# Kernel tuning notes

Measured on AMD Instinct MI355X. Metric: run time of the kernel, lower is better.

The kernel has to match this reference:

```python
import jax, jax.numpy as jnp
import numpy as np

B, T, A_DIM, Z_DIM, K = 128, 80, 32, 64, 16


def setup_inputs() -> dict:
    key = jax.random.key(0)
    k1, k2, k3, k4 = jax.random.split(key, 4)
    obs = jax.random.normal(k1, (B, T, A_DIM), jnp.float32)
    alpha_logits = jax.random.normal(k2, (B, T, K), jnp.float32)
    # torch init: A = eye(z) repeated K times; small noise keeps 80-step recursion stable
    A_K = jnp.eye(Z_DIM, dtype=jnp.float32)[None] + 0.005 * jax.random.normal(k3, (K, Z_DIM, Z_DIM), jnp.float32)
    # torch init: C = 0.05 * randn
    C_K = 0.05 * jax.random.normal(k4, (K, A_DIM, Z_DIM), jnp.float32)
    return {"obs": obs, "alpha_logits": alpha_logits, "A_K": A_K, "C_K": C_K}


def _kalman(obs, A, C):
    # obs [B,T,a], A [B,T,z,z], C [B,T,a,z]
    Bq, Tq, a_dim = obs.shape
    z_dim = A.shape[-1]
    dt = obs.dtype
    Q = 0.08 * jnp.eye(z_dim, dtype=dt)
    R = 0.03 * jnp.eye(a_dim, dtype=dt)
    I = jnp.eye(z_dim, dtype=dt)

    obs_t = jnp.swapaxes(obs, 0, 1)          # [T,B,a]
    A_t = jnp.swapaxes(A, 0, 1)              # [T,B,z,z]
    C_t = jnp.swapaxes(C, 0, 1)              # [T,B,a,z]
    A_next = jnp.concatenate([A_t[1:], A_t[-1:]], axis=0)  # A[t+1]; last unused

    mu0 = jnp.zeros((Bq, z_dim), dt)
    sig0 = jnp.broadcast_to(20.0 * I, (Bq, z_dim, z_dim))

    def filt_step(carry, inp):
        mu_p, sig_p, mu_prev = carry
        At, Anx, Ct, y = inp
        CtT = jnp.swapaxes(Ct, -1, -2)
        S = Ct @ sig_p @ CtT + R                       # [B,a,a]
        Kg = sig_p @ CtT @ jnp.linalg.inv(S)            # [B,z,a]
        Amu = jnp.einsum('bij,bj->bi', At, mu_prev)     # A_t mu_{t-1}
        err = y - jnp.einsum('bij,bj->bi', Ct, Amu)
        mu_f = Amu + jnp.einsum('bij,bj->bi', Kg, err)
        sig_f = (I - Kg @ Ct) @ sig_p
        mu_pn = jnp.einsum('bij,bj->bi', Anx, mu_f)     # prediction with A_{t+1}
        sig_pn = Anx @ sig_f @ jnp.swapaxes(Anx, -1, -2) + Q
        return (mu_pn, sig_pn, mu_f), (mu_f, sig_f, mu_p, sig_p)

    _, (mu_f, sig_f, mu_p, sig_p) = jax.lax.scan(
        filt_step, (mu0, sig0, mu0), (A_t, A_next, C_t, obs_t))

    def smooth_step(carry, inp):
        mu_s, sig_s = carry
        mf, sf, Anx, mpn, spn = inp
        J = sf @ jnp.swapaxes(Anx, -1, -2) @ jnp.linalg.inv(spn)
        mu = mf + jnp.einsum('bij,bj->bi', J, mu_s - mpn)
        sig = sf + J @ (sig_s - spn) @ jnp.swapaxes(J, -1, -2)
        return (mu, sig), (mu, sig)

    init = (mu_f[-1], sig_f[-1])
    _, (mu_sm, sig_sm) = jax.lax.scan(
        smooth_step, init,
        (mu_f[:-1], sig_f[:-1], A_t[1:], mu_p[1:], sig_p[1:]),
        reverse=True)
    mu_sm = jnp.concatenate([mu_sm, mu_f[-1:]], axis=0)
    sig_sm = jnp.concatenate([sig_sm, sig_f[-1:]], axis=0)
    return jnp.swapaxes(mu_sm, 0, 1), jnp.swapaxes(sig_sm, 0, 1)  # [B,T,z], [B,T,z,z]


def reference(obs, alpha_logits, A_K, C_K):
    w = jax.nn.softmax(alpha_logits, axis=-1)                # [B,T,K]
    A = jnp.einsum('btk,kij->btij', w, A_K)                  # [B,T,z,z]
    C = jnp.einsum('btk,kij->btij', w, C_K)                  # [B,T,a,z]
    return _kalman(obs, A, C)
```

## Files before the change

### kernel.cpp

```cpp
#include <hip/hip_runtime.h>

#define B_ 128
#define T_ 80
#define AD 32
#define ZD 64
#define KD 16
#define S8 68
#define S4 34

template<int KL, int AS, int BS, bool ATRANS>
__device__ __forceinline__ void mm64(const float* __restrict__ Pa, const float* __restrict__ Qb,
                                     float acc[2][4], int r2, int c4)
{
#pragma unroll 8
    for (int k = 0; k < KL; k++) {
        float aA, aB;
        if (ATRANS) { aA = Pa[k * AS + r2];   aB = Pa[k * AS + r2 + 1]; }
        else        { aA = Pa[r2 * AS + k];   aB = Pa[(r2 + 1) * AS + k]; }
        const float4 bv = *(const float4*)&Qb[k * BS + c4];
        acc[0][0] += aA * bv.x; acc[0][1] += aA * bv.y; acc[0][2] += aA * bv.z; acc[0][3] += aA * bv.w;
        acc[1][0] += aB * bv.x; acc[1][1] += aB * bv.y; acc[1][2] += aB * bv.z; acc[1][3] += aB * bv.w;
    }
}

__global__ __launch_bounds__(512, 2)
void kvae_kernel(const float* __restrict__ obs, const float* __restrict__ logits,
                 const float* __restrict__ AK, const float* __restrict__ CK,
                 float* __restrict__ out)
{
    __shared__ __align__(16) float W[T_ * KD];
    __shared__ __align__(16) float Am[ZD * S8];
    __shared__ __align__(16) float At[ZD * S8];
    __shared__ __align__(16) float SP[ZD * S8];
    __shared__ __align__(16) float SF[ZD * S8];
    __shared__ __align__(16) float Mm[ZD * S8];
    __shared__ __align__(16) float Pool[9792];
    __shared__ __align__(16) float y_s[32];
    __shared__ __align__(16) float mup[64];
    __shared__ __align__(16) float muf[64];
    __shared__ __align__(16) float mus[64];
    __shared__ __align__(16) float mpn[64];
    __shared__ __align__(16) float dv[64];

    float* T1 = Pool;
    float* CM = Pool + 2176;
    float* CT = Pool + 4352;
    float* U_ = Pool + 6528;
    float* S_ = Pool + 8704;
    float* Xb = Pool;
    float* SG = Pool + 4352;

    const int tid = threadIdx.x;
    const int b   = blockIdx.x;

    const int r16 = tid >> 4;
    const int cg  = tid & 15;
    const int c4  = cg << 2;
    const int c2  = cg << 1;
    const int r2  = r16 << 1;
    const int i64 = tid >> 3;
    const int c8  = (tid & 7) << 3;

    const float* obs_b = obs    + (size_t)b * T_ * AD;
    const float* lg_b  = logits + (size_t)b * T_ * KD;
    float* omu = out + (size_t)b * T_ * ZD;
    float* osg = out + (size_t)B_ * T_ * ZD + (size_t)b * T_ * ZD * ZD;
    const float4* AK4 = (const float4*)AK;
    const float4* CK4 = (const float4*)CK;

    auto mixA_full = [&](int tt) {
#pragma unroll
        for (int rr = 0; rr < 2; rr++) {
            int r = r2 + rr;
            float4 a = make_float4(0.f, 0.f, 0.f, 0.f);
#pragma unroll
            for (int k = 0; k < KD; k++) {
                float wk = W[tt * KD + k];
                float4 v = AK4[k * 1024 + r * 16 + cg];
                a.x += wk * v.x; a.y += wk * v.y; a.z += wk * v.z; a.w += wk * v.w;
            }
            *(float4*)&Am[r * S8 + c4] = a;
            At[(c4 + 0) * S8 + r] = a.x; At[(c4 + 1) * S8 + r] = a.y;
            At[(c4 + 2) * S8 + r] = a.z; At[(c4 + 3) * S8 + r] = a.w;
        }
    };
    auto mixC_full = [&](int tt) {
        float4 a = make_float4(0.f, 0.f, 0.f, 0.f);
#pragma unroll
        for (int k = 0; k < KD; k++) {
            float wk = W[tt * KD + k];
            float4 v = CK4[k * 512 + r16 * 16 + cg];
            a.x += wk * v.x; a.y += wk * v.y; a.z += wk * v.z; a.w += wk * v.w;
        }
        *(float4*)&CM[r16 * S8 + c4] = a;
        CT[(c4 + 0) * S4 + r16] = a.x; CT[(c4 + 1) * S4 + r16] = a.y;
        CT[(c4 + 2) * S4 + r16] = a.z; CT[(c4 + 3) * S4 + r16] = a.w;
    };

    if (tid < T_) {
        float l[KD]; float mx = -1e30f;
#pragma unroll
        for (int k = 0; k < KD; k++) { l[k] = lg_b[tid * KD + k]; mx = fmaxf(mx, l[k]); }
        float s = 0.f;
#pragma unroll
        for (int k = 0; k < KD; k++) { l[k] = expf(l[k] - mx); s += l[k]; }
        float inv = 1.0f / s;
#pragma unroll
        for (int k = 0; k < KD; k++) W[tid * KD + k] = l[k] * inv;
    }
#pragma unroll
    for (int rr = 0; rr < 2; rr++) {
        int r = r2 + rr;
#pragma unroll
        for (int j = 0; j < 4; j++) SP[r * S8 + c4 + j] = (r == c4 + j) ? 20.0f : 0.0f;
    }
    if (tid < ZD) mup[tid] = 0.0f;
    __syncthreads();

    for (int t = 0; t < T_; t++) {
        if (t < T_ - 1) mixA_full(t + 1);
        mixC_full(t);
        if (tid < AD) y_s[tid] = obs_b[t * AD + tid];
        __syncthreads();

        {
            float a0 = 0, a1 = 0, a2 = 0, a3 = 0;
            const float* pa = CM + r16 * S8;
#pragma unroll 8
            for (int k = 0; k < ZD; k++) {
                float a = pa[k];
                float4 bv = *(const float4*)&SP[k * S8 + c4];
                a0 += a * bv.x; a1 += a * bv.y; a2 += a * bv.z; a3 += a * bv.w;
            }
            T1[r16 * S8 + c4 + 0] = a0; T1[r16 * S8 + c4 + 1] = a1;
            T1[r16 * S8 + c4 + 2] = a2; T1[r16 * S8 + c4 + 3] = a3;
        }
        __syncthreads();

        float4 ur; float ue = 0.f;
        {
            float a0 = 0, a1 = 0;
            const float* pa = T1 + r16 * S8;
#pragma unroll 8
            for (int k = 0; k < ZD; k++) {
                float a = pa[k];
                float2 bv = *(const float2*)&CT[k * S4 + c2];
                a0 += a * bv.x; a1 += a * bv.y;
            }
            if (r16 == c2)     a0 += 0.03f;
            if (r16 == c2 + 1) a1 += 0.03f;
            S_[r16 * S4 + c2] = a0; S_[r16 * S4 + c2 + 1] = a1;
            ur = *(const float4*)&T1[r16 * S8 + c4];
            if (cg == 15) {
                float s = 0.f;
                const float* pc = CM + r16 * S8;
#pragma unroll 8
                for (int k = 0; k < ZD; k++) s += pc[k] * mup[k];
                ue = y_s[r16] - s;
            }
            if (r16 < 2) {
                *(float4*)&U_[r16 * S8 + c4] = ur;
                if (cg == 15) U_[r16 * S8 + 64] = ue;
            }
        }
        __syncthreads();

#pragma unroll 1
        for (int j = 0; j < 16; j++) {
            const int p0 = 2 * j, p1 = p0 + 1;
            const int i = r16;
            const float f0 = S_[i * S4 + p0], f1 = S_[i * S4 + p1];
            const float qa = S_[p0 * S4 + p0], qb = S_[p0 * S4 + p1];
            const float qc = S_[p1 * S4 + p0], qd = S_[p1 * S4 + p1];
            const float l0x = S_[p0 * S4 + c2], l0y = S_[p0 * S4 + c2 + 1];
            const float l1x = S_[p1 * S4 + c2], l1y = S_[p1 * S4 + c2 + 1];
            const float4 r0 = *(const float4*)&U_[p0 * S8 + c4];
            const float4 r1 = *(const float4*)&U_[p1 * S8 + c4];
            float e0 = 0.f, e1 = 0.f;
            if (cg == 15) { e0 = U_[p0 * S8 + 64]; e1 = U_[p1 * S8 + 64]; }
            __syncthreads();
            const float dinv = 1.0f / (qa * qd - qb * qc);
            const float i00 =  qd * dinv, i01 = -qb * dinv;
            const float i10 = -qc * dinv, i11 =  qa * dinv;
            const float n0x = i00 * l0x + i01 * l1x, n0y = i00 * l0y + i01 * l1y;
            const float n1x = i10 * l0x + i11 * l1x, n1y = i10 * l0y + i11 * l1y;
            float4 m0, m1;
            m0.x = i00 * r0.x + i01 * r1.x; m0.y = i00 * r0.y + i01 * r1.y;
            m0.z = i00 * r0.z + i01 * r1.z; m0.w = i00 * r0.w + i01 * r1.w;
            m1.x = i10 * r0.x + i11 * r1.x; m1.y = i10 * r0.y + i11 * r1.y;
            m1.z = i10 * r0.z + i11 * r1.z; m1.w = i10 * r0.w + i11 * r1.w;
            const float me0 = i00 * e0 + i01 * e1, me1 = i10 * e0 + i11 * e1;
            if (i == p0) {
                S_[i * S4 + c2] = n0x; S_[i * S4 + c2 + 1] = n0y;
                ur = m0; if (cg == 15) ue = me0;
            } else if (i == p1) {
                S_[i * S4 + c2] = n1x; S_[i * S4 + c2 + 1] = n1y;
                ur = m1; if (cg == 15) ue = me1;
            } else {
                S_[i * S4 + c2]     -= f0 * n0x + f1 * n1x;
                S_[i * S4 + c2 + 1] -= f0 * n0y + f1 * n1y;
                ur.x -= f0 * m0.x + f1 * m1.x; ur.y -= f0 * m0.y + f1 * m1.y;
                ur.z -= f0 * m0.z + f1 * m1.z; ur.w -= f0 * m0.w + f1 * m1.w;
                if (cg == 15) ue -= f0 * me0 + f1 * me1;
            }
            if (j < 15 && (i == p0 + 2 || i == p0 + 3)) {
                *(float4*)&U_[i * S8 + c4] = ur;
                if (cg == 15) U_[i * S8 + 64] = ue;
            }
            __syncthreads();
        }
        *(float4*)&U_[r16 * S8 + c4] = ur;
        if (cg == 15) U_[r16 * S8 + 64] = ue;
        __syncthreads();

        {
            float acc[2][4] = {};
            mm64<AD, S8, S8, true>(T1, U_, acc, r2, c4);
            float* og = osg + (size_t)t * ZD * ZD;
#pragma unroll
            for (int rr = 0; rr < 2; rr++) {
                int r = r2 + rr;
                float4 sp = *(const float4*)&SP[r * S8 + c4];
                float4 v;
                v.x = sp.x - acc[rr][0]; v.y = sp.y - acc[rr][1];
                v.z = sp.z - acc[rr][2]; v.w = sp.w - acc[rr][3];
                *(float4*)&SF[r * S8 + c4] = v;
                *(float4*)(og + r * ZD + c4) = v;
            }
        }
        if (tid < ZD) {
            float s = 0.f;
#pragma unroll
            for (int k = 0; k < AD; k++) s += T1[k * S8 + tid] * U_[k * S8 + 64];
            float v = mup[tid] + s;
            muf[tid] = v;
            omu[t * ZD + tid] = v;
        }
        __syncthreads();

        if (t < T_ - 1) {
            {
                float acc[2][4] = {};
                mm64<ZD, S8, S8, false>(Am, SF, acc, r2, c4);
#pragma unroll
                for (int rr = 0; rr < 2; rr++)
                    *(float4*)&Mm[(r2 + rr) * S8 + c4] =
                        make_float4(acc[rr][0], acc[rr][1], acc[rr][2], acc[rr][3]);
            }
            __syncthreads();
            {
                float acc[2][4] = {};
                mm64<ZD, S8, S8, false>(Mm, At, acc, r2, c4);
#pragma unroll
                for (int rr = 0; rr < 2; rr++) {
                    int r = r2 + rr;
#pragma unroll
                    for (int j = 0; j < 4; j++)
                        SP[r * S8 + c4 + j] = acc[rr][j] + ((r == c4 + j) ? 0.08f : 0.0f);
                }
            }
            if (tid >= 448) {
                int i = tid - 448;
                float s = 0.f;
                const float* pa = Am + i * S8;
#pragma unroll 8
                for (int k = 0; k < ZD; k++) s += pa[k] * muf[k];
                mup[i] = s;
            }
            __syncthreads();
        }
    }

#pragma unroll
    for (int rr = 0; rr < 2; rr++) {
        int r = r2 + rr;
        *(float4*)&SG[r * S8 + c4] = *(const float4*)&SF[r * S8 + c4];
    }
    if (tid < ZD) mus[tid] = muf[tid];
    __syncthreads();

    for (int t = T_ - 2; t >= 0; t--) {
        mixA_full(t + 1);
        {
            const float4* og4 = (const float4*)(osg + (size_t)t * ZD * ZD);
#pragma unroll
            for (int rr = 0; rr < 2; rr++) {
                int r = r2 + rr;
                *(float4*)&SF[r * S8 + c4] = og4[r * 16 + cg];
            }
        }
        if (tid >= 448) muf[tid - 448] = omu[t * ZD + (tid - 448)];
        __syncthreads();

        {
            float acc[2][4] = {};
            mm64<ZD, S8, S8, false>(Am, SF, acc, r2, c4);
#pragma unroll
            for (int rr = 0; rr < 2; rr++) {
                int r = r2 + rr;
                float4 v = make_float4(acc[rr][0], acc[rr][1], acc[rr][2], acc[rr][3]);
                *(float4*)&Mm[r * S8 + c4] = v;
                *(float4*)&Xb[r * S8 + c4] = v;
            }
        }
        if (tid >= 448) {
            int i = tid - 448;
            float s = 0.f;
            const float* pa = Am + i * S8;
#pragma unroll 8
            for (int k = 0; k < ZD; k++) s += pa[k] * muf[k];
            mpn[i] = s;
        }
        __syncthreads();

        {
            float acc[2][4] = {};
            mm64<ZD, S8, S8, false>(Mm, At, acc, r2, c4);
#pragma unroll
            for (int rr = 0; rr < 2; rr++) {
                int r = r2 + rr;
#pragma unroll
                for (int j = 0; j < 4; j++)
                    SP[r * S8 + c4 + j] = acc[rr][j] + ((r == c4 + j) ? 0.08f : 0.0f);
            }
        }
        if (tid >= 448) { int i = tid - 448; dv[i] = mus[i] - mpn[i]; }
        __syncthreads();

        float4 xr0 = *(const float4*)&Xb[i64 * S8 + c8];
        float4 xr1 = *(const float4*)&Xb[i64 * S8 + c8 + 4];
#pragma unroll 1
        for (int j = 0; j < 32; j++) {
            const int p0 = 2 * j, p1 = p0 + 1;
            const float f0 = SP[i64 * S8 + p0], f1 = SP[i64 * S8 + p1];
            const float qa = SP[p0 * S8 + p0], qb = SP[p0 * S8 + p1];
            const float qc = SP[p1 * S8 + p0], qd = SP[p1 * S8 + p1];
            const float4 l0a = *(const float4*)&SP[p0 * S8 + c8];
            const float4 l0b = *(const float4*)&SP[p0 * S8 + c8 + 4];
            const float4 l1a = *(const float4*)&SP[p1 * S8 + c8];
            const float4 l1b = *(const float4*)&SP[p1 * S8 + c8 + 4];
            const float4 r0a = *(const float4*)&Xb[p0 * S8 + c8];
            const float4 r0b = *(const float4*)&Xb[p0 * S8 + c8 + 4];
            const float4 r1a = *(const float4*)&Xb[p1 * S8 + c8];
            const float4 r1b = *(const float4*)&Xb[p1 * S8 + c8 + 4];
            const float4 ol0 = *(const float4*)&SP[i64 * S8 + c8];
            const float4 ol1 = *(const float4*)&SP[i64 * S8 + c8 + 4];
            __syncthreads();
            const float dinv = 1.0f / (qa * qd - qb * qc);
            const float i00 =  qd * dinv, i01 = -qb * dinv;
            const float i10 = -qc * dinv, i11 =  qa * dinv;
            float4 nl0a, nl0b, nl1a, nl1b, nr0a, nr0b, nr1a, nr1b;
            nl0a.x = i00*l0a.x + i01*l1a.x; nl0a.y = i00*l0a.y + i01*l1a.y;
            nl0a.z = i00*l0a.z + i01*l1a.z; nl0a.w = i00*l0a.w + i01*l1a.w;
            nl0b.x = i00*l0b.x + i01*l1b.x; nl0b.y = i00*l0b.y + i01*l1b.y;
            nl0b.z = i00*l0b.z + i01*l1b.z; nl0b.w = i00*l0b.w + i01*l1b.w;
            nl1a.x = i10*l0a.x + i11*l1a.x; nl1a.y = i10*l0a.y + i11*l1a.y;
            nl1a.z = i10*l0a.z + i11*l1a.z; nl1a.w = i10*l0a.w + i11*l1a.w;
            nl1b.x = i10*l0b.x + i11*l1b.x; nl1b.y = i10*l0b.y + i11*l1b.y;
            nl1b.z = i10*l0b.z + i11*l1b.z; nl1b.w = i10*l0b.w + i11*l1b.w;
            nr0a.x = i00*r0a.x + i01*r1a.x; nr0a.y = i00*r0a.y + i01*r1a.y;
            nr0a.z = i00*r0a.z + i01*r1a.z; nr0a.w = i00*r0a.w + i01*r1a.w;
            nr0b.x = i00*r0b.x + i01*r1b.x; nr0b.y = i00*r0b.y + i01*r1b.y;
            nr0b.z = i00*r0b.z + i01*r1b.z; nr0b.w = i00*r0b.w + i01*r1b.w;
            nr1a.x = i10*r0a.x + i11*r1a.x; nr1a.y = i10*r0a.y + i11*r1a.y;
            nr1a.z = i10*r0a.z + i11*r1a.z; nr1a.w = i10*r0a.w + i11*r1a.w;
            nr1b.x = i10*r0b.x + i11*r1b.x; nr1b.y = i10*r0b.y + i11*r1b.y;
            nr1b.z = i10*r0b.z + i11*r1b.z; nr1b.w = i10*r0b.w + i11*r1b.w;
            if (i64 == p0) {
                *(float4*)&SP[i64 * S8 + c8]     = nl0a;
                *(float4*)&SP[i64 * S8 + c8 + 4] = nl0b;
                xr0 = nr0a; xr1 = nr0b;
            } else if (i64 == p1) {
                *(float4*)&SP[i64 * S8 + c8]     = nl1a;
                *(float4*)&SP[i64 * S8 + c8 + 4] = nl1b;
                xr0 = nr1a; xr1 = nr1b;
            } else {
                float4 w0 = ol0, w1 = ol1;
                w0.x -= f0*nl0a.x + f1*nl1a.x; w0.y -= f0*nl0a.y + f1*nl1a.y;
                w0.z -= f0*nl0a.z + f1*nl1a.z; w0.w -= f0*nl0a.w + f1*nl1a.w;
                w1.x -= f0*nl0b.x + f1*nl1b.x; w1.y -= f0*nl0b.y + f1*nl1b.y;
                w1.z -= f0*nl0b.z + f1*nl1b.z; w1.w -= f0*nl0b.w + f1*nl1b.w;
                *(float4*)&SP[i64 * S8 + c8]     = w0;
                *(float4*)&SP[i64 * S8 + c8 + 4] = w1;
                xr0.x -= f0*nr0a.x + f1*nr1a.x; xr0.y -= f0*nr0a.y + f1*nr1a.y;
                xr0.z -= f0*nr0a.z + f1*nr1a.z; xr0.w -= f0*nr0a.w + f1*nr1a.w;
                xr1.x -= f0*nr0b.x + f1*nr1b.x; xr1.y -= f0*nr0b.y + f1*nr1b.y;
                xr1.z -= f0*nr0b.z + f1*nr1b.z; xr1.w -= f0*nr0b.w + f1*nr1b.w;
            }
            if (j < 31 && (i64 == p0 + 2 || i64 == p0 + 3)) {
                *(float4*)&Xb[i64 * S8 + c8]     = xr0;
                *(float4*)&Xb[i64 * S8 + c8 + 4] = xr1;
            }
            __syncthreads();
        }
        *(float4*)&Xb[i64 * S8 + c8]     = xr0;
        *(float4*)&Xb[i64 * S8 + c8 + 4] = xr1;
        __syncthreads();

        {
            float acc[2][4] = {};
            mm64<ZD, S8, S8, false>(SG, Xb, acc, r2, c4);
#pragma unroll
            for (int rr = 0; rr < 2; rr++) {
                int r = r2 + rr;
                float4 m = *(const float4*)&Mm[r * S8 + c4];
                SP[r * S8 + c4 + 0] = acc[rr][0] - m.x;
                SP[r * S8 + c4 + 1] = acc[rr][1] - m.y;
                SP[r * S8 + c4 + 2] = acc[rr][2] - m.z;
                SP[r * S8 + c4 + 3] = acc[rr][3] - m.w;
            }
        }
        __syncthreads();

        {
            float acc[2][4] = {};
            mm64<ZD, S8, S8, true>(Xb, SP, acc, r2, c4);
            float* og = osg + (size_t)t * ZD * ZD;
#pragma unroll
            for (int rr = 0; rr < 2; rr++) {
                int r = r2 + rr;
                float4 sf = *(const float4*)&SF[r * S8 + c4];
                float4 v;
                v.x = sf.x + acc[rr][0]; v.y = sf.y + acc[rr][1];
                v.z = sf.z + acc[rr][2]; v.w = sf.w + acc[rr][3];
                *(float4*)&SG[r * S8 + c4] = v;
                *(float4*)(og + r * ZD + c4) = v;
            }
        }
        if (tid < ZD) {
            float s = 0.f;
#pragma unroll 8
            for (int k = 0; k < ZD; k++) s += Xb[k * S8 + tid] * dv[k];
            float v = muf[tid] + s;
            mus[tid] = v;
            omu[t * ZD + tid] = v;
        }
        __syncthreads();
    }
}

extern "C" void kernel_launch(void* const* d_in, const int* in_sizes, int n_in,
                              void* d_out, int out_size, void* d_ws, size_t ws_size,
                              hipStream_t stream) {
    const float* obs = (const float*)d_in[0];
    const float* lg  = (const float*)d_in[1];
    const float* AK  = (const float*)d_in[2];
    const float* CK  = (const float*)d_in[3];
    (void)d_ws; (void)ws_size; (void)in_sizes; (void)n_in; (void)out_size;
    kvae_kernel<<<dim3(B_), dim3(512), 0, stream>>>(obs, lg, AK, CK, (float*)d_out);
}
```

Baseline: 3.979 ms.

## Use 4x4 block Gauss-Jordan pivots to halve barrier count in matrix solves

Replaces the 2x2-pivot Gauss-Jordan elimination for both the S (32x32) and smoother (64x64) solves with 4x4 block pivots. Each pivot block is inverted redundantly per thread through a closed-form Schur-complement formula, and pivot rows are staged in double-buffered shared arrays. This halves the number of elimination steps and their __syncthreads barriers. It adds more shared memory and per-thread arithmetic, and unpivoted 4x4 inversion may be less numerically robust.

```diff
diff --git a/kernel.cpp b/kernel.cpp
--- a/kernel.cpp
+++ b/kernel.cpp
@@ -6,7 +6,42 @@
 #define ZD 64
 #define KD 16
 #define S8 68
-#define S4 34
+#define SC 36
+
+__device__ __forceinline__ float4 ld4(const float* p) { return *(const float4*)p; }
+__device__ __forceinline__ void st4f(float* p, float4 v) { *(float4*)p = v; }
+
+__device__ __forceinline__ float4 comb4(float4 c, float4 x0, float4 x1, float4 x2, float4 x3) {
+    return make_float4(c.x*x0.x + c.y*x1.x + c.z*x2.x + c.w*x3.x,
+                       c.x*x0.y + c.y*x1.y + c.z*x2.y + c.w*x3.y,
+                       c.x*x0.z + c.y*x1.z + c.z*x2.z + c.w*x3.z,
+                       c.x*x0.w + c.y*x1.w + c.z*x2.w + c.w*x3.w);
+}
+
+__device__ __forceinline__ void pinv4(float4 q0, float4 q1, float4 q2, float4 q3,
+                                      float4& pi0, float4& pi1, float4& pi2, float4& pi3)
+{
+    const float ra = 1.0f / (q0.x*q1.y - q0.y*q1.x);
+    const float ai00 =  q1.y*ra, ai01 = -q0.y*ra, ai10 = -q1.x*ra, ai11 = q0.x*ra;
+    const float ca00 = q2.x*ai00 + q2.y*ai10, ca01 = q2.x*ai01 + q2.y*ai11;
+    const float ca10 = q3.x*ai00 + q3.y*ai10, ca11 = q3.x*ai01 + q3.y*ai11;
+    const float s00 = q2.z - (ca00*q0.z + ca01*q1.z), s01 = q2.w - (ca00*q0.w + ca01*q1.w);
+    const float s10 = q3.z - (ca10*q0.z + ca11*q1.z), s11 = q3.w - (ca10*q0.w + ca11*q1.w);
+    const float rs = 1.0f / (s00*s11 - s01*s10);
+    const float si00 = s11*rs, si01 = -s01*rs, si10 = -s10*rs, si11 = s00*rs;
+    const float ab00 = ai00*q0.z + ai01*q1.z, ab01 = ai00*q0.w + ai01*q1.w;
+    const float ab10 = ai10*q0.z + ai11*q1.z, ab11 = ai10*q0.w + ai11*q1.w;
+    const float t00 = ab00*si00 + ab01*si10, t01 = ab00*si01 + ab01*si11;
+    const float t10 = ab10*si00 + ab11*si10, t11 = ab10*si01 + ab11*si11;
+    const float tl00 = ai00 + (t00*ca00 + t01*ca10), tl01 = ai01 + (t00*ca01 + t01*ca11);
+    const float tl10 = ai10 + (t10*ca00 + t11*ca10), tl11 = ai11 + (t10*ca01 + t11*ca11);
+    const float bl00 = -(si00*ca00 + si01*ca10), bl01 = -(si00*ca01 + si01*ca11);
+    const float bl10 = -(si10*ca00 + si11*ca10), bl11 = -(si10*ca01 + si11*ca11);
+    pi0 = make_float4(tl00, tl01, -t00, -t01);
+    pi1 = make_float4(tl10, tl11, -t10, -t11);
+    pi2 = make_float4(bl00, bl01, si00, si01);
+    pi3 = make_float4(bl10, bl11, si10, si11);
+}
 
 template<int KL, int AS, int BS, bool ATRANS>
 __device__ __forceinline__ void mm64(const float* __restrict__ Pa, const float* __restrict__ Qb,
@@ -17,7 +52,7 @@
         float aA, aB;
         if (ATRANS) { aA = Pa[k * AS + r2];   aB = Pa[k * AS + r2 + 1]; }
         else        { aA = Pa[r2 * AS + k];   aB = Pa[(r2 + 1) * AS + k]; }
-        const float4 bv = *(const float4*)&Qb[k * BS + c4];
+        const float4 bv = ld4(&Qb[k * BS + c4]);
         acc[0][0] += aA * bv.x; acc[0][1] += aA * bv.y; acc[0][2] += aA * bv.z; acc[0][3] += aA * bv.w;
         acc[1][0] += aB * bv.x; acc[1][1] += aB * bv.y; acc[1][2] += aB * bv.z; acc[1][3] += aB * bv.w;
     }
@@ -34,8 +69,14 @@
     __shared__ __align__(16) float SP[ZD * S8];
     __shared__ __align__(16) float SF[ZD * S8];
     __shared__ __align__(16) float Mm[ZD * S8];
-    __shared__ __align__(16) float Pool[9792];
+    __shared__ __align__(16) float Pool[9984];
+    __shared__ __align__(16) float pvL[512];
+    __shared__ __align__(16) float pvR[512];
+    __shared__ __align__(16) float fbb[512];
+    __shared__ __align__(16) float pvE[8];
     __shared__ __align__(16) float y_s[32];
+    __shared__ __align__(16) float errv[32];
+    __shared__ __align__(16) float uev[32];
     __shared__ __align__(16) float mup[64];
     __shared__ __align__(16) float muf[64];
     __shared__ __align__(16) float mus[64];
@@ -45,8 +86,8 @@
     float* T1 = Pool;
     float* CM = Pool + 2176;
     float* CT = Pool + 4352;
-    float* U_ = Pool + 6528;
-    float* S_ = Pool + 8704;
+    float* U_ = Pool + 6656;
+    float* S_ = Pool + 8832;
     float* Xb = Pool;
     float* SG = Pool + 4352;
 
@@ -58,8 +99,8 @@
     const int c4  = cg << 2;
     const int c2  = cg << 1;
     const int r2  = r16 << 1;
-    const int i64 = tid >> 3;
-    const int c8  = (tid & 7) << 3;
+    const int gi  = tid >> 3;
+    const int gs  = tid & 7;
 
     const float* obs_b = obs    + (size_t)b * T_ * AD;
     const float* lg_b  = logits + (size_t)b * T_ * KD;
@@ -68,33 +109,33 @@
     const float4* AK4 = (const float4*)AK;
     const float4* CK4 = (const float4*)CK;
 
-    auto mixA_full = [&](int tt) {
+    auto mixA = [&](int tt) {
 #pragma unroll
         for (int rr = 0; rr < 2; rr++) {
-            int r = r2 + rr;
+            const int r = r2 + rr;
             float4 a = make_float4(0.f, 0.f, 0.f, 0.f);
 #pragma unroll
             for (int k = 0; k < KD; k++) {
-                float wk = W[tt * KD + k];
-                float4 v = AK4[k * 1024 + r * 16 + cg];
+                const float wk = W[tt * KD + k];
+                const float4 v = AK4[k * 1024 + r * 16 + cg];
                 a.x += wk * v.x; a.y += wk * v.y; a.z += wk * v.z; a.w += wk * v.w;
             }
-            *(float4*)&Am[r * S8 + c4] = a;
+            st4f(&Am[r * S8 + c4], a);
             At[(c4 + 0) * S8 + r] = a.x; At[(c4 + 1) * S8 + r] = a.y;
             At[(c4 + 2) * S8 + r] = a.z; At[(c4 + 3) * S8 + r] = a.w;
         }
     };
-    auto mixC_full = [&](int tt) {
+    auto mixC = [&](int tt) {
         float4 a = make_float4(0.f, 0.f, 0.f, 0.f);
 #pragma unroll
         for (int k = 0; k < KD; k++) {
-            float wk = W[tt * KD + k];
-            float4 v = CK4[k * 512 + r16 * 16 + cg];
+            const float wk = W[tt * KD + k];
+            const float4 v = CK4[k * 512 + r16 * 16 + cg];
             a.x += wk * v.x; a.y += wk * v.y; a.z += wk * v.z; a.w += wk * v.w;
         }
-        *(float4*)&CM[r16 * S8 + c4] = a;
-        CT[(c4 + 0) * S4 + r16] = a.x; CT[(c4 + 1) * S4 + r16] = a.y;
-        CT[(c4 + 2) * S4 + r16] = a.z; CT[(c4 + 3) * S4 + r16] = a.w;
+        st4f(&CM[r16 * S8 + c4], a);
+        CT[(c4 + 0) * SC + r16] = a.x; CT[(c4 + 1) * SC + r16] = a.y;
+        CT[(c4 + 2) * SC + r16] = a.z; CT[(c4 + 3) * SC + r16] = a.w;
     };
 
     if (tid < T_) {
@@ -104,13 +145,13 @@
         float s = 0.f;
 #pragma unroll
         for (int k = 0; k < KD; k++) { l[k] = expf(l[k] - mx); s += l[k]; }
-        float inv = 1.0f / s;
+        const float inv = 1.0f / s;
 #pragma unroll
         for (int k = 0; k < KD; k++) W[tid * KD + k] = l[k] * inv;
     }
 #pragma unroll
     for (int rr = 0; rr < 2; rr++) {
-        int r = r2 + rr;
+        const int r = r2 + rr;
 #pragma unroll
         for (int j = 0; j < 4; j++) SP[r * S8 + c4 + j] = (r == c4 + j) ? 20.0f : 0.0f;
     }
@@ -118,8 +159,8 @@
     __syncthreads();
 
     for (int t = 0; t < T_; t++) {
-        if (t < T_ - 1) mixA_full(t + 1);
-        mixC_full(t);
+        if (t < T_ - 1) mixA(t + 1);
+        mixC(t);
         if (tid < AD) y_s[tid] = obs_b[t * AD + tid];
         __syncthreads();
 
@@ -128,8 +169,8 @@
             const float* pa = CM + r16 * S8;
 #pragma unroll 8
             for (int k = 0; k < ZD; k++) {
-                float a = pa[k];
-                float4 bv = *(const float4*)&SP[k * S8 + c4];
+                const float a = pa[k];
+                const float4 bv = ld4(&SP[k * S8 + c4]);
                 a0 += a * bv.x; a1 += a * bv.y; a2 += a * bv.z; a3 += a * bv.w;
             }
             T1[r16 * S8 + c4 + 0] = a0; T1[r16 * S8 + c4 + 1] = a1;
@@ -137,80 +178,97 @@
         }
         __syncthreads();
 
-        float4 ur; float ue = 0.f;
         {
             float a0 = 0, a1 = 0;
             const float* pa = T1 + r16 * S8;
 #pragma unroll 8
             for (int k = 0; k < ZD; k++) {
-                float a = pa[k];
-                float2 bv = *(const float2*)&CT[k * S4 + c2];
+                const float a = pa[k];
+                const float2 bv = *(const float2*)&CT[k * SC + c2];
                 a0 += a * bv.x; a1 += a * bv.y;
             }
             if (r16 == c2)     a0 += 0.03f;
             if (r16 == c2 + 1) a1 += 0.03f;
-            S_[r16 * S4 + c2] = a0; S_[r16 * S4 + c2 + 1] = a1;
-            ur = *(const float4*)&T1[r16 * S8 + c4];
-            if (cg == 15) {
-                float s = 0.f;
-                const float* pc = CM + r16 * S8;
-#pragma unroll 8
-                for (int k = 0; k < ZD; k++) s += pc[k] * mup[k];
-                ue = y_s[r16] - s;
-            }
-            if (r16 < 2) {
-                *(float4*)&U_[r16 * S8 + c4] = ur;
-                if (cg == 15) U_[r16 * S8 + 64] = ue;
-            }
-        }
-        __syncthreads();
-
-#pragma unroll 1
-        for (int j = 0; j < 16; j++) {
-            const int p0 = 2 * j, p1 = p0 + 1;
-            const int i = r16;
-            const float f0 = S_[i * S4 + p0], f1 = S_[i * S4 + p1];
-            const float qa = S_[p0 * S4 + p0], qb = S_[p0 * S4 + p1];
-            const float qc = S_[p1 * S4 + p0], qd = S_[p1 * S4 + p1];
-            const float l0x = S_[p0 * S4 + c2], l0y = S_[p0 * S4 + c2 + 1];
-            const float l1x = S_[p1 * S4 + c2], l1y = S_[p1 * S4 + c2 + 1];
-            const float4 r0 = *(const float4*)&U_[p0 * S8 + c4];
-            const float4 r1 = *(const float4*)&U_[p1 * S8 + c4];
-            float e0 = 0.f, e1 = 0.f;
-            if (cg == 15) { e0 = U_[p0 * S8 + 64]; e1 = U_[p1 * S8 + 64]; }
+            S_[r16 * SC + c2] = a0; S_[r16 * SC + c2 + 1] = a1;
+        }
+        if (tid < AD) {
+            float s = 0.f;
+#pragma unroll
+            for (int k4 = 0; k4 < ZD; k4 += 4) {
+                const float4 cm = ld4(&CM[tid * S8 + k4]);
+                const float4 mu = ld4(&mup[k4]);
+                s += cm.x*mu.x + cm.y*mu.y + cm.z*mu.z + cm.w*mu.w;
+            }
+            errv[tid] = y_s[tid] - s;
+        }
+        __syncthreads();
+
+        {
+            const int hi = r16, hs = cg;
+            float4 aL = make_float4(0, 0, 0, 0);
+            float4 aR = ld4(&T1[hi * S8 + hs * 4]);
+            float e = 0.f;
+            if (hs < 8) aL = ld4(&S_[hi * SC + hs * 4]);
+            if (hs == 15) e = errv[hi];
+            if (hi < 4) {
+                if (hs < 8) st4f(&pvL[hi * 32 + hs * 4], aL);
+                st4f(&pvR[hi * 64 + hs * 4], aR);
+                if (hs == 15) pvE[hi] = e;
+            }
+            if (hs == 0) st4f(&fbb[hi * 4], aL);
             __syncthreads();
-            const float dinv = 1.0f / (qa * qd - qb * qc);
-            const float i00 =  qd * dinv, i01 = -qb * dinv;
-            const float i10 = -qc * dinv, i11 =  qa * dinv;
-            const float n0x = i00 * l0x + i01 * l1x, n0y = i00 * l0y + i01 * l1y;
-            const float n1x = i10 * l0x + i11 * l1x, n1y = i10 * l0y + i11 * l1y;
-            float4 m0, m1;
-            m0.x = i00 * r0.x + i01 * r1.x; m0.y = i00 * r0.y + i01 * r1.y;
-            m0.z = i00 * r0.z + i01 * r1.z; m0.w = i00 * r0.w + i01 * r1.w;
-            m1.x = i10 * r0.x + i11 * r1.x; m1.y = i10 * r0.y + i11 * r1.y;
-            m1.z = i10 * r0.z + i11 * r1.z; m1.w = i10 * r0.w + i11 * r1.w;
-            const float me0 = i00 * e0 + i01 * e1, me1 = i10 * e0 + i11 * e1;
-            if (i == p0) {
-                S_[i * S4 + c2] = n0x; S_[i * S4 + c2 + 1] = n0y;
-                ur = m0; if (cg == 15) ue = me0;
-            } else if (i == p1) {
-                S_[i * S4 + c2] = n1x; S_[i * S4 + c2 + 1] = n1y;
-                ur = m1; if (cg == 15) ue = me1;
-            } else {
-                S_[i * S4 + c2]     -= f0 * n0x + f1 * n1x;
-                S_[i * S4 + c2 + 1] -= f0 * n0y + f1 * n1y;
-                ur.x -= f0 * m0.x + f1 * m1.x; ur.y -= f0 * m0.y + f1 * m1.y;
-                ur.z -= f0 * m0.z + f1 * m1.z; ur.w -= f0 * m0.w + f1 * m1.w;
-                if (cg == 15) ue -= f0 * me0 + f1 * me1;
-            }
-            if (j < 15 && (i == p0 + 2 || i == p0 + 3)) {
-                *(float4*)&U_[i * S8 + c4] = ur;
-                if (cg == 15) U_[i * S8 + 64] = ue;
-            }
-            __syncthreads();
-        }
-        *(float4*)&U_[r16 * S8 + c4] = ur;
-        if (cg == 15) U_[r16 * S8 + 64] = ue;
+
+#pragma unroll 2
+            for (int j = 0; j < 8; ++j) {
+                const int par = j & 1, nb = par ^ 1;
+                const bool isp = (hi >> 2) == j;
+                const float4 f  = ld4(&fbb[par * 128 + hi * 4]);
+                const float4 q0 = ld4(&fbb[par * 128 + (4 * j + 0) * 4]);
+                const float4 q1 = ld4(&fbb[par * 128 + (4 * j + 1) * 4]);
+                const float4 q2 = ld4(&fbb[par * 128 + (4 * j + 2) * 4]);
+                const float4 q3 = ld4(&fbb[par * 128 + (4 * j + 3) * 4]);
+                float4 pi0, pi1, pi2, pi3;
+                pinv4(q0, q1, q2, q3, pi0, pi1, pi2, pi3);
+                const int rr = hi & 3;
+                const float4 coef = isp ? (rr == 0 ? pi0 : rr == 1 ? pi1 : rr == 2 ? pi2 : pi3)
+                                        : comb4(f, pi0, pi1, pi2, pi3);
+                {
+                    const float4 x0 = ld4(&pvR[par * 256 + 0 * 64 + hs * 4]);
+                    const float4 x1 = ld4(&pvR[par * 256 + 1 * 64 + hs * 4]);
+                    const float4 x2 = ld4(&pvR[par * 256 + 2 * 64 + hs * 4]);
+                    const float4 x3 = ld4(&pvR[par * 256 + 3 * 64 + hs * 4]);
+                    const float4 c = comb4(coef, x0, x1, x2, x3);
+                    if (isp) aR = c;
+                    else { aR.x -= c.x; aR.y -= c.y; aR.z -= c.z; aR.w -= c.w; }
+                }
+                if (hs < 8) {
+                    const float4 x0 = ld4(&pvL[par * 128 + 0 * 32 + hs * 4]);
+                    const float4 x1 = ld4(&pvL[par * 128 + 1 * 32 + hs * 4]);
+                    const float4 x2 = ld4(&pvL[par * 128 + 2 * 32 + hs * 4]);
+                    const float4 x3 = ld4(&pvL[par * 128 + 3 * 32 + hs * 4]);
+                    const float4 c = comb4(coef, x0, x1, x2, x3);
+                    if (isp) aL = c;
+                    else { aL.x -= c.x; aL.y -= c.y; aL.z -= c.z; aL.w -= c.w; }
+                }
+                if (hs == 15) {
+                    const float e0 = pvE[par * 4 + 0], e1 = pvE[par * 4 + 1];
+                    const float e2 = pvE[par * 4 + 2], e3 = pvE[par * 4 + 3];
+                    const float ce = coef.x * e0 + coef.y * e1 + coef.z * e2 + coef.w * e3;
+                    if (isp) e = ce; else e -= ce;
+                }
+                if (j < 7) {
+                    if ((hi >> 2) == j + 1) {
+                        if (hs < 8) st4f(&pvL[nb * 128 + (hi & 3) * 32 + hs * 4], aL);
+                        st4f(&pvR[nb * 256 + (hi & 3) * 64 + hs * 4], aR);
+                        if (hs == 15) pvE[nb * 4 + (hi & 3)] = e;
+                    }
+                    if (hs == j + 1) st4f(&fbb[nb * 128 + hi * 4], aL);
+                }
+                __syncthreads();
+            }
+            st4f(&U_[hi * S8 + hs * 4], aR);
+            if (hs == 15) uev[hi] = e;
+        }
         __syncthreads();
 
         {
@@ -219,20 +277,19 @@
             float* og = osg + (size_t)t * ZD * ZD;
 #pragma unroll
             for (int rr = 0; rr < 2; rr++) {
-                int r = r2 + rr;
-                float4 sp = *(const float4*)&SP[r * S8 + c4];
-                float4 v;
-                v.x = sp.x - acc[rr][0]; v.y = sp.y - acc[rr][1];
-                v.z = sp.z - acc[rr][2]; v.w = sp.w - acc[rr][3];
-                *(float4*)&SF[r * S8 + c4] = v;
+                const int r = r2 + rr;
+                const float4 sp = ld4(&SP[r * S8 + c4]);
+                const float4 v = make_float4(sp.x - acc[rr][0], sp.y - acc[rr][1],
+                                             sp.z - acc[rr][2], sp.w - acc[rr][3]);
+                st4f(&SF[r * S8 + c4], v);
                 *(float4*)(og + r * ZD + c4) = v;
             }
         }
         if (tid < ZD) {
             float s = 0.f;
 #pragma unroll
-            for (int k = 0; k < AD; k++) s += T1[k * S8 + tid] * U_[k * S8 + 64];
-            float v = mup[tid] + s;
+            for (int k = 0; k < AD; k++) s += T1[k * S8 + tid] * uev[k];
+            const float v = mup[tid] + s;
             muf[tid] = v;
             omu[t * ZD + tid] = v;
         }
@@ -244,8 +301,8 @@
                 mm64<ZD, S8, S8, false>(Am, SF, acc, r2, c4);
 #pragma unroll
                 for (int rr = 0; rr < 2; rr++)
-                    *(float4*)&Mm[(r2 + rr) * S8 + c4] =
-                        make_float4(acc[rr][0], acc[rr][1], acc[rr][2], acc[rr][3]);
+                    st4f(&Mm[(r2 + rr) * S8 + c4],
+                         make_float4(acc[rr][0], acc[rr][1], acc[rr][2], acc[rr][3]));
             }
             __syncthreads();
             {
@@ -253,14 +310,14 @@
                 mm64<ZD, S8, S8, false>(Mm, At, acc, r2, c4);
 #pragma unroll
                 for (int rr = 0; rr < 2; rr++) {
-                    int r = r2 + rr;
+                    const int r = r2 + rr;
 #pragma unroll
                     for (int j = 0; j < 4; j++)
                         SP[r * S8 + c4 + j] = acc[rr][j] + ((r == c4 + j) ? 0.08f : 0.0f);
                 }
             }
             if (tid >= 448) {
-                int i = tid - 448;
+                const int i = tid - 448;
                 float s = 0.f;
                 const float* pa = Am + i * S8;
 #pragma unroll 8
@@ -272,22 +329,18 @@
     }
 
 #pragma unroll
-    for (int rr = 0; rr < 2; rr++) {
-        int r = r2 + rr;
-        *(float4*)&SG[r * S8 + c4] = *(const float4*)&SF[r * S8 + c4];
-    }
+    for (int rr = 0; rr < 2; rr++)
+        st4f(&SG[(r2 + rr) * S8 + c4], ld4(&SF[(r2 + rr) * S8 + c4]));
     if (tid < ZD) mus[tid] = muf[tid];
     __syncthreads();
 
     for (int t = T_ - 2; t >= 0; t--) {
-        mixA_full(t + 1);
+        mixA(t + 1);
         {
             const float4* og4 = (const float4*)(osg + (size_t)t * ZD * ZD);
 #pragma unroll
-            for (int rr = 0; rr < 2; rr++) {
-                int r = r2 + rr;
-                *(float4*)&SF[r * S8 + c4] = og4[r * 16 + cg];
-            }
+            for (int rr = 0; rr < 2; rr++)
+                st4f(&SF[(r2 + rr) * S8 + c4], og4[(r2 + rr) * 16 + cg]);
         }
         if (tid >= 448) muf[tid - 448] = omu[t * ZD + (tid - 448)];
         __syncthreads();
@@ -296,15 +349,12 @@
             float acc[2][4] = {};
             mm64<ZD, S8, S8, false>(Am, SF, acc, r2, c4);
 #pragma unroll
-            for (int rr = 0; rr < 2; rr++) {
-                int r = r2 + rr;
-                float4 v = make_float4(acc[rr][0], acc[rr][1], acc[rr][2], acc[rr][3]);
-                *(float4*)&Mm[r * S8 + c4] = v;
-                *(float4*)&Xb[r * S8 + c4] = v;
-            }
+            for (int rr = 0; rr < 2; rr++)
+                st4f(&Mm[(r2 + rr) * S8 + c4],
+                     make_float4(acc[rr][0], acc[rr][1], acc[rr][2], acc[rr][3]));
         }
         if (tid >= 448) {
-            int i = tid - 448;
+            const int i = tid - 448;
             float s = 0.f;
             const float* pa = Am + i * S8;
 #pragma unroll 8
@@ -318,83 +368,93 @@
             mm64<ZD, S8, S8, false>(Mm, At, acc, r2, c4);
 #pragma unroll
             for (int rr = 0; rr < 2; rr++) {
-                int r = r2 + rr;
+                const int r = r2 + rr;
 #pragma unroll
                 for (int j = 0; j < 4; j++)
                     SP[r * S8 + c4 + j] = acc[rr][j] + ((r == c4 + j) ? 0.08f : 0.0f);
             }
         }
-        if (tid >= 448) { int i = tid - 448; dv[i] = mus[i] - mpn[i]; }
-        __syncthreads();
-
-        float4 xr0 = *(const float4*)&Xb[i64 * S8 + c8];
-        float4 xr1 = *(const float4*)&Xb[i64 * S8 + c8 + 4];
-#pragma unroll 1
-        for (int j = 0; j < 32; j++) {
-            const int p0 = 2 * j, p1 = p0 + 1;
-            const float f0 = SP[i64 * S8 + p0], f1 = SP[i64 * S8 + p1];
-            const float qa = SP[p0 * S8 + p0], qb = SP[p0 * S8 + p1];
-            const float qc = SP[p1 * S8 + p0], qd = SP[p1 * S8 + p1];
-            const float4 l0a = *(const float4*)&SP[p0 * S8 + c8];
-            const float4 l0b = *(const float4*)&SP[p0 * S8 + c8 + 4];
-            const float4 l1a = *(const float4*)&SP[p1 * S8 + c8];
-            const float4 l1b = *(const float4*)&SP[p1 * S8 + c8 + 4];
-            const float4 r0a = *(const float4*)&Xb[p0 * S8 + c8];
-            const float4 r0b = *(const float4*)&Xb[p0 * S8 + c8 + 4];
-            const float4 r1a = *(const float4*)&Xb[p1 * S8 + c8];
-            const float4 r1b = *(const float4*)&Xb[p1 * S8 + c8 + 4];
-            const float4 ol0 = *(const float4*)&SP[i64 * S8 + c8];
-            const float4 ol1 = *(const float4*)&SP[i64 * S8 + c8 + 4];
+        if (tid >= 448) { const int i = tid - 448; dv[i] = mus[i] - mpn[i]; }
+        __syncthreads();
+
+        {
+            float4 aL0 = ld4(&SP[gi * S8 + gs * 8]);
+            float4 aL1 = ld4(&SP[gi * S8 + gs * 8 + 4]);
+            float4 aR0 = ld4(&Mm[gi * S8 + gs * 8]);
+            float4 aR1 = ld4(&Mm[gi * S8 + gs * 8 + 4]);
+            if (gi < 4) {
+                st4f(&pvL[gi * 64 + gs * 8], aL0); st4f(&pvL[gi * 64 + gs * 8 + 4], aL1);
+                st4f(&pvR[gi * 64 + gs * 8], aR0); st4f(&pvR[gi * 64 + gs * 8 + 4], aR1);
+            }
+            if (gs == 0) st4f(&fbb[gi * 4], aL0);
             __syncthreads();
-            const float dinv = 1.0f / (qa * qd - qb * qc);
-            const float i00 =  qd * dinv, i01 = -qb * dinv;
-            const float i10 = -qc * dinv, i11 =  qa * dinv;
-            float4 nl0a, nl0b, nl1a, nl1b, nr0a, nr0b, nr1a, nr1b;
-            nl0a.x = i00*l0a.x + i01*l1a.x; nl0a.y = i00*l0a.y + i01*l1a.y;
-            nl0a.z = i00*l0a.z + i01*l1a.z; nl0a.w = i00*l0a.w + i01*l1a.w;
-            nl0b.x = i00*l0b.x + i01*l1b.x; nl0b.y = i00*l0b.y + i01*l1b.y;
-            nl0b.z = i00*l0b.z + i01*l1b.z; nl0b.w = i00*l0b.w + i01*l1b.w;
-            nl1a.x = i10*l0a.x + i11*l1a.x; nl1a.y = i10*l0a.y + i11*l1a.y;
-            nl1a.z = i10*l0a.z + i11*l1a.z; nl1a.w = i10*l0a.w + i11*l1a.w;
-            nl1b.x = i10*l0b.x + i11*l1b.x; nl1b.y = i10*l0b.y + i11*l1b.y;
-            nl1b.z = i10*l0b.z + i11*l1b.z; nl1b.w = i10*l0b.w + i11*l1b.w;
-            nr0a.x = i00*r0a.x + i01*r1a.x; nr0a.y = i00*r0a.y + i01*r1a.y;
-            nr0a.z = i00*r0a.z + i01*r1a.z; nr0a.w = i00*r0a.w + i01*r1a.w;
-            nr0b.x = i00*r0b.x + i01*r1b.x; nr0b.y = i00*r0b.y + i01*r1b.y;
-            nr0b.z = i00*r0b.z + i01*r1b.z; nr0b.w = i00*r0b.w + i01*r1b.w;
-            nr1a.x = i10*r0a.x + i11*r1a.x; nr1a.y = i10*r0a.y + i11*r1a.y;
-            nr1a.z = i10*r0a.z + i11*r1a.z; nr1a.w = i10*r0a.w + i11*r1a.w;
-            nr1b.x = i10*r0b.x + i11*r1b.x; nr1b.y = i10*r0b.y + i11*r1b.y;
-            nr1b.z = i10*r0b.z + i11*r1b.z; nr1b.w = i10*r0b.w + i11*r1b.w;
-            if (i64 == p0) {
-                *(float4*)&SP[i64 * S8 + c8]     = nl0a;
-                *(float4*)&SP[i64 * S8 + c8 + 4] = nl0b;
-                xr0 = nr0a; xr1 = nr0b;
-            } else if (i64 == p1) {
-                *(float4*)&SP[i64 * S8 + c8]     = nl1a;
-                *(float4*)&SP[i64 * S8 + c8 + 4] = nl1b;
-                xr0 = nr1a; xr1 = nr1b;
-            } else {
-                float4 w0 = ol0, w1 = ol1;
-                w0.x -= f0*nl0a.x + f1*nl1a.x; w0.y -= f0*nl0a.y + f1*nl1a.y;
-                w0.z -= f0*nl0a.z + f1*nl1a.z; w0.w -= f0*nl0a.w + f1*nl1a.w;
-                w1.x -= f0*nl0b.x + f1*nl1b.x; w1.y -= f0*nl0b.y + f1*nl1b.y;
-                w1.z -= f0*nl0b.z + f1*nl1b.z; w1.w -= f0*nl0b.w + f1*nl1b.w;
-                *(float4*)&SP[i64 * S8 + c8]     = w0;
-                *(float4*)&SP[i64 * S8 + c8 + 4] = w1;
-                xr0.x -= f0*nr0a.x + f1*nr1a.x; xr0.y -= f0*nr0a.y + f1*nr1a.y;
-                xr0.z -= f0*nr0a.z + f1*nr1a.z; xr0.w -= f0*nr0a.w + f1*nr1a.w;
-                xr1.x -= f0*nr0b.x + f1*nr1b.x; xr1.y -= f0*nr0b.y + f1*nr1b.y;
-                xr1.z -= f0*nr0b.z + f1*nr1b.z; xr1.w -= f0*nr0b.w + f1*nr1b.w;
-            }
-            if (j < 31 && (i64 == p0 + 2 || i64 == p0 + 3)) {
-                *(float4*)&Xb[i64 * S8 + c8]     = xr0;
-                *(float4*)&Xb[i64 * S8 + c8 + 4] = xr1;
-            }
-            __syncthreads();
-        }
-        *(float4*)&Xb[i64 * S8 + c8]     = xr0;
-        *(float4*)&Xb[i64 * S8 + c8 + 4] = xr1;
+
+#pragma unroll 2
+            for (int j = 0; j < 16; ++j) {
+                const int par = j & 1, nb = par ^ 1;
+                const bool isp = (gi >> 2) == j;
+                const float4 f  = ld4(&fbb[par * 256 + gi * 4]);
+                const float4 q0 = ld4(&fbb[par * 256 + (4 * j + 0) * 4]);
+                const float4 q1 = ld4(&fbb[par * 256 + (4 * j + 1) * 4]);
+                const float4 q2 = ld4(&fbb[par * 256 + (4 * j + 2) * 4]);
+                const float4 q3 = ld4(&fbb[par * 256 + (4 * j + 3) * 4]);
+                float4 pi0, pi1, pi2, pi3;
+                pinv4(q0, q1, q2, q3, pi0, pi1, pi2, pi3);
+                const int rr = gi & 3;
+                const float4 coef = isp ? (rr == 0 ? pi0 : rr == 1 ? pi1 : rr == 2 ? pi2 : pi3)
+                                        : comb4(f, pi0, pi1, pi2, pi3);
+                {
+                    const float4 x0 = ld4(&pvL[par * 256 + 0 * 64 + gs * 8]);
+                    const float4 x1 = ld4(&pvL[par * 256 + 1 * 64 + gs * 8]);
+                    const float4 x2 = ld4(&pvL[par * 256 + 2 * 64 + gs * 8]);
+                    const float4 x3 = ld4(&pvL[par * 256 + 3 * 64 + gs * 8]);
+                    const float4 c = comb4(coef, x0, x1, x2, x3);
+                    if (isp) aL0 = c;
+                    else { aL0.x -= c.x; aL0.y -= c.y; aL0.z -= c.z; aL0.w -= c.w; }
+                }
+                {
+                    const float4 x0 = ld4(&pvL[par * 256 + 0 * 64 + gs * 8 + 4]);
+                    const float4 x1 = ld4(&pvL[par * 256 + 1 * 64 + gs * 8 + 4]);
+                    const float4 x2 = ld4(&pvL[par * 256 + 2 * 64 + gs * 8 + 4]);
+                    const float4 x3 = ld4(&pvL[par * 256 + 3 * 64 + gs * 8 + 4]);
+                    const float4 c = comb4(coef, x0, x1, x2, x3);
+                    if (isp) aL1 = c;
+                    else { aL1.x -= c.x; aL1.y -= c.y; aL1.z -= c.z; aL1.w -= c.w; }
+                }
+                {
+                    const float4 x0 = ld4(&pvR[par * 256 + 0 * 64 + gs * 8]);
+                    const float4 x1 = ld4(&pvR[par * 256 + 1 * 64 + gs * 8]);
+                    const float4 x2 = ld4(&pvR[par * 256 + 2 * 64 + gs * 8]);
+                    const float4 x3 = ld4(&pvR[par * 256 + 3 * 64 + gs * 8]);
+                    const float4 c = comb4(coef, x0, x1, x2, x3);
+                    if (isp) aR0 = c;
+                    else { aR0.x -= c.x; aR0.y -= c.y; aR0.z -= c.z; aR0.w -= c.w; }
+                }
+                {
+                    const float4 x0 = ld4(&pvR[par * 256 + 0 * 64 + gs * 8 + 4]);
+                    const float4 x1 = ld4(&pvR[par * 256 + 1 * 64 + gs * 8 + 4]);
+                    const float4 x2 = ld4(&pvR[par * 256 + 2 * 64 + gs * 8 + 4]);
+                    const float4 x3 = ld4(&pvR[par * 256 + 3 * 64 + gs * 8 + 4]);
+                    const float4 c = comb4(coef, x0, x1, x2, x3);
+                    if (isp) aR1 = c;
+                    else { aR1.x -= c.x; aR1.y -= c.y; aR1.z -= c.z; aR1.w -= c.w; }
+                }
+                if (j < 15) {
+                    if ((gi >> 2) == j + 1) {
+                        const int rn = gi & 3;
+                        st4f(&pvL[nb * 256 + rn * 64 + gs * 8], aL0);
+                        st4f(&pvL[nb * 256 + rn * 64 + gs * 8 + 4], aL1);
+                        st4f(&pvR[nb * 256 + rn * 64 + gs * 8], aR0);
+                        st4f(&pvR[nb * 256 + rn * 64 + gs * 8 + 4], aR1);
+                    }
+                    if (gs == ((j + 1) >> 1))
+                        st4f(&fbb[nb * 256 + gi * 4], ((j + 1) & 1) ? aL1 : aL0);
+                }
+                __syncthreads();
+            }
+            st4f(&Xb[gi * S8 + gs * 8], aR0);
+            st4f(&Xb[gi * S8 + gs * 8 + 4], aR1);
+        }
         __syncthreads();
 
         {
@@ -402,8 +462,8 @@
             mm64<ZD, S8, S8, false>(SG, Xb, acc, r2, c4);
 #pragma unroll
             for (int rr = 0; rr < 2; rr++) {
-                int r = r2 + rr;
-                float4 m = *(const float4*)&Mm[r * S8 + c4];
+                const int r = r2 + rr;
+                const float4 m = ld4(&Mm[r * S8 + c4]);
                 SP[r * S8 + c4 + 0] = acc[rr][0] - m.x;
                 SP[r * S8 + c4 + 1] = acc[rr][1] - m.y;
                 SP[r * S8 + c4 + 2] = acc[rr][2] - m.z;
@@ -418,12 +478,11 @@
             float* og = osg + (size_t)t * ZD * ZD;
 #pragma unroll
             for (int rr = 0; rr < 2; rr++) {
-                int r = r2 + rr;
-                float4 sf = *(const float4*)&SF[r * S8 + c4];
-                float4 v;
-                v.x = sf.x + acc[rr][0]; v.y = sf.y + acc[rr][1];
-                v.z = sf.z + acc[rr][2]; v.w = sf.w + acc[rr][3];
-                *(float4*)&SG[r * S8 + c4] = v;
+                const int r = r2 + rr;
+                const float4 sf = ld4(&SF[r * S8 + c4]);
+                const float4 v = make_float4(sf.x + acc[rr][0], sf.y + acc[rr][1],
+                                             sf.z + acc[rr][2], sf.w + acc[rr][3]);
+                st4f(&SG[r * S8 + c4], v);
                 *(float4*)(og + r * ZD + c4) = v;
             }
         }
@@ -431,7 +490,7 @@
             float s = 0.f;
 #pragma unroll 8
             for (int k = 0; k < ZD; k++) s += Xb[k * S8 + tid] * dv[k];
-            float v = muf[tid] + s;
+            const float v = muf[tid] + s;
             mus[tid] = v;
             omu[t * ZD + tid] = v;
         }
```

New measurement: 3.609 ms. 9.3% less time.
